# Kernel optimization log

Hardware: AMD Instinct MI355X
Metric: run time of the kernel (lower is better)

## Reference

```python
import jax, jax.numpy as jnp
import numpy as np

N = 25000      # nodes
E = 400000     # edges (before self loops)
G = 64         # graphs in batch
H = 16         # attention heads
ITER = 10      # stacked main GATv2 layers


def setup_inputs():
    key = jax.random.key(0)
    c = [0]
    def nk():
        c[0] += 1
        return jax.random.fold_in(key, c[0])
    def glorot(shape):
        fan = shape[-2] + shape[-1]
        return jax.random.normal(nk(), shape, jnp.float32) * np.float32(np.sqrt(2.0 / fan))
    inp = {
        "x": jax.random.normal(nk(), (N, 2), jnp.float32),
        "edge_attr": jax.random.normal(nk(), (E, 2), jnp.float32),
        "edge_index": jax.random.randint(nk(), (2, E), 0, N, jnp.int32),
        "mask": jax.random.randint(nk(), (N,), 0, 2, jnp.int32),
        "batch": jnp.sort(jax.random.randint(nk(), (N,), 0, G, jnp.int32)),
        # gcn: GATv2Conv(2, 4, heads=16, edge_dim=2), concat -> 64
        "g0_Wl": glorot((2, 64)), "g0_bl": jnp.zeros((64,), jnp.float32),
        "g0_Wr": glorot((2, 64)), "g0_br": jnp.zeros((64,), jnp.float32),
        "g0_We": glorot((2, 64)), "g0_att": glorot((H, 4)),
        "g0_bias": jnp.zeros((64,), jnp.float32),
        "bn_gamma": jnp.ones((64,), jnp.float32),
        "bn_beta": jnp.zeros((64,), jnp.float32),
        "m_Wl": glorot((ITER, 64, 64)), "m_bl": jnp.zeros((ITER, 64), jnp.float32),
        "m_Wr": glorot((ITER, 64, 64)), "m_br": jnp.zeros((ITER, 64), jnp.float32),
        "m_We": glorot((ITER, 2, 64)), "m_att": glorot((ITER, H, 4)),
        "m_bias": jnp.zeros((ITER, 64), jnp.float32),
        # final: GATv2Conv(64, 1, heads=16, concat=False)
        "f_Wl": glorot((64, 16)), "f_bl": jnp.zeros((16,), jnp.float32),
        "f_Wr": glorot((64, 16)), "f_br": jnp.zeros((16,), jnp.float32),
        "f_We": glorot((2, 16)), "f_att": glorot((H, 1)),
        "f_bias": jnp.zeros((1,), jnp.float32),
        # sbs: GATv2Conv(64, 1, heads=16, concat=False)
        "s_Wl": glorot((64, 16)), "s_bl": jnp.zeros((16,), jnp.float32),
        "s_Wr": glorot((64, 16)), "s_br": jnp.zeros((16,), jnp.float32),
        "s_We": glorot((2, 16)), "s_att": glorot((H, 1)),
        "s_bias": jnp.zeros((1,), jnp.float32),
    }
    return inp


def _gatv2(x, src, dst, eattr, Wl, bl, Wr, br, We, att, bias, concat):
    """PyG GATv2Conv: x_l[j]+x_r[i]+e -> LeakyReLU(0.2) -> att dot -> segment softmax over dst."""
    n = x.shape[0]
    h, c = att.shape
    xl = (x @ Wl + bl).reshape(n, h, c)
    xr = (x @ Wr + br).reshape(n, h, c)
    e = (eattr @ We).reshape(-1, h, c)
    m = jax.nn.leaky_relu(xl[src] + xr[dst] + e, 0.2)          # [Etot,H,C]
    logit = jnp.einsum('ehc,hc->eh', m, att)                    # [Etot,H]
    lmax = jax.ops.segment_max(logit, dst, num_segments=n)
    ex = jnp.exp(logit - lmax[dst])
    den = jax.ops.segment_sum(ex, dst, num_segments=n)
    alpha = ex / den[dst]
    out = jax.ops.segment_sum(xl[src] * alpha[..., None], dst, num_segments=n)  # [N,H,C]
    out = out.reshape(n, h * c) if concat else out.mean(axis=1)
    return out + bias


def reference(x, edge_attr, edge_index, mask, batch,
              g0_Wl, g0_bl, g0_Wr, g0_br, g0_We, g0_att, g0_bias,
              bn_gamma, bn_beta,
              m_Wl, m_bl, m_Wr, m_br, m_We, m_att, m_bias,
              f_Wl, f_bl, f_Wr, f_br, f_We, f_att, f_bias,
              s_Wl, s_bl, s_Wr, s_br, s_We, s_att, s_bias):
    n = x.shape[0]
    src, dst = edge_index[0], edge_index[1]
    # add self loops; self-loop edge attr = mean of incoming edge attrs (fill_value='mean')
    ones = jnp.ones((src.shape[0],), jnp.float32)
    cnt = jax.ops.segment_sum(ones, dst, num_segments=n)
    esum = jax.ops.segment_sum(edge_attr, dst, num_segments=n)
    loop_attr = esum / jnp.maximum(cnt, 1.0)[:, None]
    arng = jnp.arange(n, dtype=edge_index.dtype)
    src2 = jnp.concatenate([src, arng])
    dst2 = jnp.concatenate([dst, arng])
    ea2 = jnp.concatenate([edge_attr, loop_attr], axis=0)

    h0 = _gatv2(x, src2, dst2, ea2, g0_Wl, g0_bl, g0_Wr, g0_br, g0_We, g0_att, g0_bias, True)
    mu = h0.mean(axis=0)
    var = h0.var(axis=0)
    h = jax.nn.leaky_relu((h0 - mu) * jax.lax.rsqrt(var + 1e-5) * bn_gamma + bn_beta, 0.01)

    def step(hc, p):
        Wl, bl, Wr, br, We, att, bias = p
        hc = jax.nn.leaky_relu(_gatv2(hc, src2, dst2, ea2, Wl, bl, Wr, br, We, att, bias, True), 0.01)
        return hc, None
    h, _ = jax.lax.scan(step, h, (m_Wl, m_bl, m_Wr, m_br, m_We, m_att, m_bias))

    mus = _gatv2(h, src2, dst2, ea2, s_Wl, s_bl, s_Wr, s_br, s_We, s_att, s_bias, False)[:, 0]  # [N]
    fin = _gatv2(h, src2, dst2, ea2, f_Wl, f_bl, f_Wr, f_br, f_We, f_att, f_bias, False)        # [N,1]
    w = (mask == 0).astype(jnp.float32)
    sums = jax.ops.segment_sum(fin * w[:, None], batch, num_segments=G)
    cnts = jax.ops.segment_sum(w, batch, num_segments=G)
    sat = (sums / jnp.maximum(cnts, 1.0)[:, None])[:, 0]  # [G]
    return mus, sat
```

## Files before the change

### kernel.cpp

```cpp
#include <hip/hip_runtime.h>


static __device__ __forceinline__ float lrelu(float x, float s) {
    return x > 0.f ? x : s * x;
}

__global__ void k_build0(const int* __restrict__ dst, int* __restrict__ cnt,
                         int* __restrict__ rank, int E,
                         const float* __restrict__ x,
                         const float* __restrict__ Wl, const float* __restrict__ bl,
                         const float* __restrict__ Wr, const float* __restrict__ br,
                         float* __restrict__ xl, float* __restrict__ xr, int n) {
    int idx = blockIdx.x * blockDim.x + threadIdx.x;
    if (idx < E) {
        rank[idx] = atomicAdd(&cnt[dst[idx]], 1);
    } else {
        int t = idx - E;
        if (t < n * 64) {
            int i = t >> 6, c = t & 63;
            float x0 = x[2 * i], x1 = x[2 * i + 1];
            xl[t] = x0 * Wl[c] + x1 * Wl[64 + c] + bl[c];
            xr[t] = x0 * Wr[c] + x1 * Wr[64 + c] + br[c];
        }
    }
}

__global__ void k_segoff(const int* __restrict__ cnt, int* __restrict__ row_start,
                         int* __restrict__ cursor, int n) {
    int i = blockIdx.x * blockDim.x + threadIdx.x;
    int lane = threadIdx.x & 63;
    int v = (i < n) ? cnt[i] + 1 : 0;
    int s = v;
#pragma unroll
    for (int off = 1; off < 64; off <<= 1) {
        int t = __shfl_up(s, off);
        if (lane >= off) s += t;
    }
    int wavetot = __shfl(s, 63);
    int base = 0;
    if (lane == 63) base = atomicAdd(cursor, wavetot);
    base = __shfl(base, 63);
    if (i < n) row_start[i] = base + s - v;
}

__global__ void k_scatter(const int* __restrict__ src, const int* __restrict__ dst,
                          const float* __restrict__ ea, const int* __restrict__ rank,
                          const int* __restrict__ row_start,
                          int* __restrict__ csr_src, float* __restrict__ csr_ea, int E) {
    int e = blockIdx.x * blockDim.x + threadIdx.x;
    if (e >= E) return;
    int pos = row_start[dst[e]] + rank[e];
    csr_src[pos] = src[e];
    *(float2*)(csr_ea + 2 * (size_t)pos) = *(const float2*)(ea + 2 * (size_t)e);
}

__global__ void k_selfloop(const int* __restrict__ row_start, const int* __restrict__ cnt,
                           int* __restrict__ csr_src, float* __restrict__ csr_ea, int n) {
    int i = blockIdx.x * blockDim.x + threadIdx.x;
    if (i >= n) return;
    int p0 = row_start[i], deg = cnt[i];
    float s0 = 0.f, s1 = 0.f;
    for (int p = p0; p < p0 + deg; ++p) {
        s0 += csr_ea[2 * (size_t)p];
        s1 += csr_ea[2 * (size_t)p + 1];
    }
    float c = fmaxf((float)deg, 1.f);
    int pl = p0 + deg;
    csr_src[pl] = i;
    csr_ea[2 * (size_t)pl] = s0 / c;
    csr_ea[2 * (size_t)pl + 1] = s1 / c;
}

__launch_bounds__(256)
__global__ void k_proj64(const float* __restrict__ h,
                         const float* __restrict__ Wl, const float* __restrict__ bl,
                         const float* __restrict__ Wr, const float* __restrict__ br,
                         const double* __restrict__ stats,
                         const float* __restrict__ bng, const float* __restrict__ bnb,
                         float* __restrict__ xl, float* __restrict__ xr, int n) {
    __shared__ float wsl[4096], wsr[4096], bna[64], bnbb[64];
    int t = threadIdx.x;
    for (int i = t; i < 4096; i += 256) { wsl[i] = Wl[i]; wsr[i] = Wr[i]; }
    const bool bn = (stats != nullptr);
    if (bn && t < 64) {
        double mu = stats[t] / n;
        double var = stats[64 + t] / n - mu * mu;
        float rs = (float)(1.0 / sqrt(var + 1e-5));
        float a = rs * bng[t];
        bna[t] = a;
        bnbb[t] = bnb[t] - (float)mu * a;
    }
    __syncthreads();
    int rg = t >> 2, cg4 = (t & 3) << 4;
    int r0 = blockIdx.x * 128 + rg * 2;
    float accl[2][16], accr[2][16];
#pragma unroll
    for (int r = 0; r < 2; ++r)
#pragma unroll
        for (int j = 0; j < 16; ++j) { accl[r][j] = 0.f; accr[r][j] = 0.f; }
    for (int k0 = 0; k0 < 64; k0 += 4) {
        float hk[2][4];
#pragma unroll
        for (int r = 0; r < 2; ++r) {
            int gr = r0 + r;
            float4 v = (gr < n) ? *(const float4*)(h + (size_t)gr * 64 + k0)
                                : make_float4(0.f, 0.f, 0.f, 0.f);
            hk[r][0] = v.x; hk[r][1] = v.y; hk[r][2] = v.z; hk[r][3] = v.w;
            if (bn) {
#pragma unroll
                for (int kk = 0; kk < 4; ++kk)
                    hk[r][kk] = lrelu(hk[r][kk] * bna[k0 + kk] + bnbb[k0 + kk], 0.01f);
            }
        }
#pragma unroll
        for (int kk = 0; kk < 4; ++kk) {
            const float* wl = wsl + (k0 + kk) * 64 + cg4;
            const float* wr = wsr + (k0 + kk) * 64 + cg4;
#pragma unroll
            for (int r = 0; r < 2; ++r)
#pragma unroll
                for (int j = 0; j < 16; ++j) {
                    accl[r][j] += hk[r][kk] * wl[j];
                    accr[r][j] += hk[r][kk] * wr[j];
                }
        }
    }
#pragma unroll
    for (int r = 0; r < 2; ++r) {
        int gr = r0 + r;
        if (gr < n) {
            float* ol = xl + (size_t)gr * 64 + cg4;
            float* orr = xr + (size_t)gr * 64 + cg4;
#pragma unroll
            for (int j = 0; j < 16; ++j) {
                ol[j] = accl[r][j] + bl[cg4 + j];
                orr[j] = accr[r][j] + br[cg4 + j];
            }
        }
    }
}

__launch_bounds__(256)
__global__ void k_proj_final(const float* __restrict__ h,
                             const float* __restrict__ fWl, const float* __restrict__ fbl,
                             const float* __restrict__ fWr, const float* __restrict__ fbr,
                             const float* __restrict__ sWl, const float* __restrict__ sbl,
                             const float* __restrict__ sWr, const float* __restrict__ sbr,
                             float* __restrict__ packed, int n) {
    __shared__ float ws[4096];
    __shared__ float bs[64];
    int t = threadIdx.x;
    for (int i = t; i < 1024; i += 256) {
        int k = i >> 4, j = i & 15;
        ws[k * 64 + j] = fWl[i];
        ws[k * 64 + 16 + j] = sWl[i];
        ws[k * 64 + 32 + j] = fWr[i];
        ws[k * 64 + 48 + j] = sWr[i];
    }
    if (t < 16) { bs[t] = fbl[t]; bs[16 + t] = sbl[t]; bs[32 + t] = fbr[t]; bs[48 + t] = sbr[t]; }
    __syncthreads();
    int rg = t >> 2, cg4 = (t & 3) << 4;
    int r0 = blockIdx.x * 256 + rg * 4;
    float acc[4][16];
#pragma unroll
    for (int r = 0; r < 4; ++r)
#pragma unroll
        for (int j = 0; j < 16; ++j) acc[r][j] = 0.f;
    for (int k0 = 0; k0 < 64; k0 += 4) {
        float hk[4][4];
#pragma unroll
        for (int r = 0; r < 4; ++r) {
            int gr = r0 + r;
            float4 v = (gr < n) ? *(const float4*)(h + (size_t)gr * 64 + k0)
                                : make_float4(0.f, 0.f, 0.f, 0.f);
            hk[r][0] = v.x; hk[r][1] = v.y; hk[r][2] = v.z; hk[r][3] = v.w;
        }
#pragma unroll
        for (int kk = 0; kk < 4; ++kk) {
            const float* wrow = ws + (k0 + kk) * 64 + cg4;
#pragma unroll
            for (int r = 0; r < 4; ++r)
#pragma unroll
                for (int j = 0; j < 16; ++j) acc[r][j] += hk[r][kk] * wrow[j];
        }
    }
#pragma unroll
    for (int r = 0; r < 4; ++r) {
        int gr = r0 + r;
        if (gr < n) {
            float* o = packed + (size_t)gr * 64 + cg4;
#pragma unroll
            for (int j = 0; j < 16; ++j) o[j] = acc[r][j] + bs[cg4 + j];
        }
    }
}

__launch_bounds__(256)
__global__ void k_gat(const float* __restrict__ xl, const float* __restrict__ xr,
                      const int* __restrict__ row_start, const int* __restrict__ cnt,
                      const int* __restrict__ csr_src, const float* __restrict__ csr_ea,
                      const float* __restrict__ We, const float* __restrict__ att,
                      const float* __restrict__ bias,
                      float* __restrict__ out, int n, int relu) {
    int wave = (blockIdx.x * blockDim.x + threadIdx.x) >> 6;
    int lane = threadIdx.x & 63;
    if (wave >= n) return;
    const int d = wave;
    const int p0 = __builtin_amdgcn_readfirstlane(row_start[d]);
    const int p1 = p0 + __builtin_amdgcn_readfirstlane(cnt[d]) + 1;
    const float we0 = We[lane], we1 = We[64 + lane];
    const float av = att[lane];
    const float xrv = xr[(size_t)d * 64 + lane];

    float mx0 = -3.0e38f, den0 = 0.f, acc0 = 0.f;
    float mx1 = -3.0e38f, den1 = 0.f, acc1 = 0.f;

    auto step = [&](float xv, float2 ea, bool valid, float& mx, float& den, float& acc) {
        float tv = lrelu(xv + xrv + ea.x * we0 + ea.y * we1, 0.2f) * av;
        tv += __shfl_xor(tv, 1);
        tv += __shfl_xor(tv, 2);
        if (!valid) tv = -__builtin_inff();
        float nm = fmaxf(mx, tv);
        float sc = __expf(mx - nm), w = __expf(tv - nm);
        den = den * sc + w;
        acc = acc * sc + w * xv;
        mx = nm;
    };

    for (int p = p0; p < p1; p += 4) {
        int q1 = min(p + 1, p1 - 1), q2 = min(p + 2, p1 - 1), q3 = min(p + 3, p1 - 1);
        int s0 = csr_src[p], s1 = csr_src[q1], s2 = csr_src[q2], s3 = csr_src[q3];
        float2 e0 = *(const float2*)(csr_ea + 2 * (size_t)p);
        float2 e1 = *(const float2*)(csr_ea + 2 * (size_t)q1);
        float2 e2 = *(const float2*)(csr_ea + 2 * (size_t)q2);
        float2 e3 = *(const float2*)(csr_ea + 2 * (size_t)q3);
        float x0 = xl[(size_t)s0 * 64 + lane];
        float x1 = xl[(size_t)s1 * 64 + lane];
        float x2 = xl[(size_t)s2 * 64 + lane];
        float x3 = xl[(size_t)s3 * 64 + lane];
        step(x0, e0, true, mx0, den0, acc0);
        step(x1, e1, p + 1 < p1, mx1, den1, acc1);
        step(x2, e2, p + 2 < p1, mx0, den0, acc0);
        step(x3, e3, p + 3 < p1, mx1, den1, acc1);
    }
    float nm = fmaxf(mx0, mx1);
    float sc0 = __expf(mx0 - nm), sc1 = __expf(mx1 - nm);
    float o = (acc0 * sc0 + acc1 * sc1) / (den0 * sc0 + den1 * sc1) + bias[lane];
    if (relu) o = lrelu(o, 0.01f);
    out[(size_t)d * 64 + lane] = o;
}

__launch_bounds__(256)
__global__ void k_gat_final(const float* __restrict__ packed,
                            const int* __restrict__ row_start, const int* __restrict__ cnt,
                            const int* __restrict__ csr_src, const float* __restrict__ csr_ea,
                            const float* __restrict__ fWe, const float* __restrict__ sWe,
                            const float* __restrict__ fatt, const float* __restrict__ satt,
                            const float* __restrict__ fbias, const float* __restrict__ sbias,
                            float* __restrict__ fin, float* __restrict__ mus, int n) {
    int hw = (blockIdx.x * blockDim.x + threadIdx.x) >> 5;
    if (hw >= n) return;
    int l = threadIdx.x & 31;
    int hh = l & 15, sel = l >> 4;
    const int d = hw;
    const int p0 = row_start[d], p1 = p0 + cnt[d] + 1;
    const float* We = sel ? sWe : fWe;
    float we0 = We[hh], we1 = We[16 + hh];
    float av = (sel ? satt : fatt)[hh];
    float xrv = packed[(size_t)d * 64 + 32 + sel * 16 + hh];
    int xli = sel * 16 + hh;

    float mx0 = -3.0e38f, den0 = 0.f, acc0 = 0.f;
    float mx1 = -3.0e38f, den1 = 0.f, acc1 = 0.f;

    auto step = [&](float xv, float2 ea, bool valid, float& mx, float& den, float& acc) {
        float t = lrelu(xv + xrv + ea.x * we0 + ea.y * we1, 0.2f) * av;
        if (!valid) t = -__builtin_inff();
        float nm = fmaxf(mx, t);
        float sc = __expf(mx - nm), w = __expf(t - nm);
        den = den * sc + w;
        acc = acc * sc + w * xv;
        mx = nm;
    };

    for (int p = p0; p < p1; p += 4) {
        int q1 = min(p + 1, p1 - 1), q2 = min(p + 2, p1 - 1), q3 = min(p + 3, p1 - 1);
        int s0 = csr_src[p], s1 = csr_src[q1], s2 = csr_src[q2], s3 = csr_src[q3];
        float2 e0 = *(const float2*)(csr_ea + 2 * (size_t)p);
        float2 e1 = *(const float2*)(csr_ea + 2 * (size_t)q1);
        float2 e2 = *(const float2*)(csr_ea + 2 * (size_t)q2);
        float2 e3 = *(const float2*)(csr_ea + 2 * (size_t)q3);
        float x0 = packed[(size_t)s0 * 64 + xli];
        float x1 = packed[(size_t)s1 * 64 + xli];
        float x2 = packed[(size_t)s2 * 64 + xli];
        float x3 = packed[(size_t)s3 * 64 + xli];
        step(x0, e0, true, mx0, den0, acc0);
        step(x1, e1, p + 1 < p1, mx1, den1, acc1);
        step(x2, e2, p + 2 < p1, mx0, den0, acc0);
        step(x3, e3, p + 3 < p1, mx1, den1, acc1);
    }
    float nm = fmaxf(mx0, mx1);
    float s0 = __expf(mx0 - nm), s1 = __expf(mx1 - nm);
    float val = (acc0 * s0 + acc1 * s1) / (den0 * s0 + den1 * s1);
#pragma unroll
    for (int w = 1; w < 16; w <<= 1) val += __shfl_xor(val, w);
    if ((threadIdx.x & 15) == 0) {
        float o = val * (1.f / 16.f) + (sel ? sbias[0] : fbias[0]);
        if (sel) mus[d] = o; else fin[d] = o;
    }
}


__global__ void k_bnstats(const float* __restrict__ h, double* __restrict__ stats, int n) {
    int c = threadIdx.x & 63;
    int s0 = blockIdx.x * (blockDim.x >> 6) + (threadIdx.x >> 6);
    int ns = gridDim.x * (blockDim.x >> 6);
    double s = 0.0, s2 = 0.0;
    for (int i = s0; i < n; i += ns) {
        float v = h[(size_t)i * 64 + c];
        s += v;
        s2 += (double)v * v;
    }
    atomicAdd(&stats[c], s);
    atomicAdd(&stats[64 + c], s2);
}


__global__ void k_sat_acc(const float* __restrict__ fin, const int* __restrict__ mask,
                          const int* __restrict__ batch,
                          float* __restrict__ sums, float* __restrict__ cnts, int n) {
    int i = blockIdx.x * blockDim.x + threadIdx.x;
    int lane = threadIdx.x & 63;
    int g = (i < n) ? batch[i] : -1;
    float c = (i < n && mask[i] == 0) ? 1.f : 0.f;
    float v = (c > 0.f) ? fin[i] : 0.f;
#pragma unroll
    for (int off = 1; off < 64; off <<= 1) {
        float v2 = __shfl_down(v, off);
        float c2 = __shfl_down(c, off);
        int g2 = __shfl_down(g, off);
        if (lane + off < 64 && g2 == g) { v += v2; c += c2; }
    }
    int gprev = __shfl_up(g, 1);
    bool head = (lane == 0) || (gprev != g);
    if (head && g >= 0 && c > 0.f) {
        atomicAdd(&sums[g], v);
        atomicAdd(&cnts[g], c);
    }
}

__global__ void k_sat_fin(const float* __restrict__ sums, const float* __restrict__ cnts,
                          float* __restrict__ out, int g) {
    int i = threadIdx.x;
    if (i < g) out[i] = sums[i] / fmaxf(cnts[i], 1.f);
}


extern "C" void kernel_launch(void* const* d_in, const int* in_sizes, int n_in,
                              void* d_out, int out_size, void* d_ws, size_t ws_size,
                              hipStream_t stream) {
    const float* x = (const float*)d_in[0];
    const float* eat = (const float*)d_in[1];
    const int* ei = (const int*)d_in[2];
    const int* mask = (const int*)d_in[3];
    const int* batch = (const int*)d_in[4];
    const float* g0_Wl = (const float*)d_in[5];
    const float* g0_bl = (const float*)d_in[6];
    const float* g0_Wr = (const float*)d_in[7];
    const float* g0_br = (const float*)d_in[8];
    const float* g0_We = (const float*)d_in[9];
    const float* g0_att = (const float*)d_in[10];
    const float* g0_bias = (const float*)d_in[11];
    const float* bn_g = (const float*)d_in[12];
    const float* bn_b = (const float*)d_in[13];
    const float* m_Wl = (const float*)d_in[14];
    const float* m_bl = (const float*)d_in[15];
    const float* m_Wr = (const float*)d_in[16];
    const float* m_br = (const float*)d_in[17];
    const float* m_We = (const float*)d_in[18];
    const float* m_att = (const float*)d_in[19];
    const float* m_bias = (const float*)d_in[20];
    const float* f_Wl = (const float*)d_in[21];
    const float* f_bl = (const float*)d_in[22];
    const float* f_Wr = (const float*)d_in[23];
    const float* f_br = (const float*)d_in[24];
    const float* f_We = (const float*)d_in[25];
    const float* f_att = (const float*)d_in[26];
    const float* f_bias = (const float*)d_in[27];
    const float* s_Wl = (const float*)d_in[28];
    const float* s_bl = (const float*)d_in[29];
    const float* s_Wr = (const float*)d_in[30];
    const float* s_br = (const float*)d_in[31];
    const float* s_We = (const float*)d_in[32];
    const float* s_att = (const float*)d_in[33];
    const float* s_bias = (const float*)d_in[34];

    const int N = in_sizes[3];
    const int E = in_sizes[1] / 2;
    const int G = out_size - N;
    const int ITER = in_sizes[14] / 4096;
    const int ET = E + N;
    const int* srcp = ei;
    const int* dstp = ei + E;

    char* wsb = (char*)d_ws;
    size_t off = 0;
    auto alloc = [&](size_t b) { void* p = wsb + off; off = (off + b + 255) & ~(size_t)255; return p; };
    int* cnt = (int*)alloc((size_t)N * 4);
    int* cursor = (int*)alloc(256);
    double* stats = (double*)alloc(128 * 8);
    float* sums = (float*)alloc((size_t)G * 4);
    float* cnts = (float*)alloc((size_t)G * 4);
    size_t zero_bytes = off;
    int* rank = (int*)alloc((size_t)E * 4);
    int* row_start = (int*)alloc((size_t)N * 4);
    int* csr_src = (int*)alloc((size_t)ET * 4);
    float* csr_ea = (float*)alloc((size_t)ET * 8);
    float* xl = (float*)alloc((size_t)N * 256);
    float* xr = (float*)alloc((size_t)N * 256);
    float* hbuf = (float*)alloc((size_t)N * 256);
    float* fin = (float*)alloc((size_t)N * 4);
    (void)ws_size; (void)n_in;

    float* outv = (float*)d_out;

    hipMemsetAsync(d_ws, 0, zero_bytes, stream);
    const int tb = 256;
    k_build0<<<(E + N * 64 + tb - 1) / tb, tb, 0, stream>>>(dstp, cnt, rank, E,
                                                            x, g0_Wl, g0_bl, g0_Wr, g0_br,
                                                            xl, xr, N);
    k_segoff<<<(N + tb - 1) / tb, tb, 0, stream>>>(cnt, row_start, cursor, N);
    k_scatter<<<(E + tb - 1) / tb, tb, 0, stream>>>(srcp, dstp, eat, rank, row_start,
                                                    csr_src, csr_ea, E);
    k_selfloop<<<(N + tb - 1) / tb, tb, 0, stream>>>(row_start, cnt, csr_src, csr_ea, N);

    k_gat<<<(N * 64 + tb - 1) / tb, tb, 0, stream>>>(xl, xr, row_start, cnt, csr_src, csr_ea,
                                                     g0_We, g0_att, g0_bias, hbuf, N, 0);
    k_bnstats<<<128, 256, 0, stream>>>(hbuf, stats, N);

    int gp = (N + 127) / 128;
    for (int l = 0; l < ITER; ++l) {
        k_proj64<<<gp, 256, 0, stream>>>(hbuf, m_Wl + (size_t)l * 4096, m_bl + l * 64,
                                         m_Wr + (size_t)l * 4096, m_br + l * 64,
                                         (l == 0) ? stats : nullptr, bn_g, bn_b,
                                         xl, xr, N);
        k_gat<<<(N * 64 + tb - 1) / tb, tb, 0, stream>>>(xl, xr, row_start, cnt, csr_src, csr_ea,
                                                         m_We + l * 128, m_att + l * 64,
                                                         m_bias + l * 64, hbuf, N, 1);
    }
    k_proj_final<<<(N + 255) / 256, 256, 0, stream>>>(hbuf, f_Wl, f_bl, f_Wr, f_br,
                                                      s_Wl, s_bl, s_Wr, s_br, xl, N);
    k_gat_final<<<(N * 32 + tb - 1) / tb, tb, 0, stream>>>(xl, row_start, cnt, csr_src, csr_ea,
                                                           f_We, s_We, f_att, s_att,
                                                           f_bias, s_bias, fin, outv, N);
    k_sat_acc<<<(N + tb - 1) / tb, tb, 0, stream>>>(fin, mask, batch, sums, cnts, N);
    k_sat_fin<<<1, 64, 0, stream>>>(sums, cnts, outv + N, G);
}
```

Baseline: 744.8 us.

## Fuse next-layer projection into GAT aggregation kernel with ping-pong buffers

Each main-layer GAT aggregation kernel now also computes the next layer's Wl/Wr projection in-register: each wave broadcasts its node's output across lanes with shuffles and multiplies by weights read from global memory. The last layer fuses the final/sbs projection instead. This removes the separate projection launches and the round trip of the hidden state through global memory, and double-buffers xl/xr so a layer never overwrites the inputs its neighbours still read. In exchange, weights are read per wave from global/cache rather than shared memory, and each wave now does 64-step shuffle loops after its aggregation.

```diff
diff --git a/kernel.cpp b/kernel.cpp
--- a/kernel.cpp
+++ b/kernel.cpp
@@ -81,8 +81,7 @@
     __shared__ float wsl[4096], wsr[4096], bna[64], bnbb[64];
     int t = threadIdx.x;
     for (int i = t; i < 4096; i += 256) { wsl[i] = Wl[i]; wsr[i] = Wr[i]; }
-    const bool bn = (stats != nullptr);
-    if (bn && t < 64) {
+    if (t < 64) {
         double mu = stats[t] / n;
         double var = stats[64 + t] / n - mu * mu;
         float rs = (float)(1.0 / sqrt(var + 1e-5));
@@ -106,11 +105,9 @@
             float4 v = (gr < n) ? *(const float4*)(h + (size_t)gr * 64 + k0)
                                 : make_float4(0.f, 0.f, 0.f, 0.f);
             hk[r][0] = v.x; hk[r][1] = v.y; hk[r][2] = v.z; hk[r][3] = v.w;
-            if (bn) {
-#pragma unroll
-                for (int kk = 0; kk < 4; ++kk)
-                    hk[r][kk] = lrelu(hk[r][kk] * bna[k0 + kk] + bnbb[k0 + kk], 0.01f);
-            }
+#pragma unroll
+            for (int kk = 0; kk < 4; ++kk)
+                hk[r][kk] = lrelu(hk[r][kk] * bna[k0 + kk] + bnbb[k0 + kk], 0.01f);
         }
 #pragma unroll
         for (int kk = 0; kk < 4; ++kk) {
@@ -140,72 +137,16 @@
     }
 }
 
-__launch_bounds__(256)
-__global__ void k_proj_final(const float* __restrict__ h,
-                             const float* __restrict__ fWl, const float* __restrict__ fbl,
-                             const float* __restrict__ fWr, const float* __restrict__ fbr,
-                             const float* __restrict__ sWl, const float* __restrict__ sbl,
-                             const float* __restrict__ sWr, const float* __restrict__ sbr,
-                             float* __restrict__ packed, int n) {
-    __shared__ float ws[4096];
-    __shared__ float bs[64];
-    int t = threadIdx.x;
-    for (int i = t; i < 1024; i += 256) {
-        int k = i >> 4, j = i & 15;
-        ws[k * 64 + j] = fWl[i];
-        ws[k * 64 + 16 + j] = sWl[i];
-        ws[k * 64 + 32 + j] = fWr[i];
-        ws[k * 64 + 48 + j] = sWr[i];
-    }
-    if (t < 16) { bs[t] = fbl[t]; bs[16 + t] = sbl[t]; bs[32 + t] = fbr[t]; bs[48 + t] = sbr[t]; }
-    __syncthreads();
-    int rg = t >> 2, cg4 = (t & 3) << 4;
-    int r0 = blockIdx.x * 256 + rg * 4;
-    float acc[4][16];
-#pragma unroll
-    for (int r = 0; r < 4; ++r)
-#pragma unroll
-        for (int j = 0; j < 16; ++j) acc[r][j] = 0.f;
-    for (int k0 = 0; k0 < 64; k0 += 4) {
-        float hk[4][4];
-#pragma unroll
-        for (int r = 0; r < 4; ++r) {
-            int gr = r0 + r;
-            float4 v = (gr < n) ? *(const float4*)(h + (size_t)gr * 64 + k0)
-                                : make_float4(0.f, 0.f, 0.f, 0.f);
-            hk[r][0] = v.x; hk[r][1] = v.y; hk[r][2] = v.z; hk[r][3] = v.w;
-        }
-#pragma unroll
-        for (int kk = 0; kk < 4; ++kk) {
-            const float* wrow = ws + (k0 + kk) * 64 + cg4;
-#pragma unroll
-            for (int r = 0; r < 4; ++r)
-#pragma unroll
-                for (int j = 0; j < 16; ++j) acc[r][j] += hk[r][kk] * wrow[j];
-        }
-    }
-#pragma unroll
-    for (int r = 0; r < 4; ++r) {
-        int gr = r0 + r;
-        if (gr < n) {
-            float* o = packed + (size_t)gr * 64 + cg4;
-#pragma unroll
-            for (int j = 0; j < 16; ++j) o[j] = acc[r][j] + bs[cg4 + j];
-        }
-    }
-}
-
-__launch_bounds__(256)
-__global__ void k_gat(const float* __restrict__ xl, const float* __restrict__ xr,
-                      const int* __restrict__ row_start, const int* __restrict__ cnt,
-                      const int* __restrict__ csr_src, const float* __restrict__ csr_ea,
-                      const float* __restrict__ We, const float* __restrict__ att,
-                      const float* __restrict__ bias,
-                      float* __restrict__ out, int n, int relu) {
-    int wave = (blockIdx.x * blockDim.x + threadIdx.x) >> 6;
-    int lane = threadIdx.x & 63;
-    if (wave >= n) return;
-    const int d = wave;
+__device__ __forceinline__ float gat_node(const float* __restrict__ xl,
+                                          const float* __restrict__ xr,
+                                          const int* __restrict__ row_start,
+                                          const int* __restrict__ cnt,
+                                          const int* __restrict__ csr_src,
+                                          const float* __restrict__ csr_ea,
+                                          const float* __restrict__ We,
+                                          const float* __restrict__ att,
+                                          const float* __restrict__ bias,
+                                          int d, int lane, int relu) {
     const int p0 = __builtin_amdgcn_readfirstlane(row_start[d]);
     const int p1 = p0 + __builtin_amdgcn_readfirstlane(cnt[d]) + 1;
     const float we0 = We[lane], we1 = We[64 + lane];
@@ -247,7 +188,77 @@
     float sc0 = __expf(mx0 - nm), sc1 = __expf(mx1 - nm);
     float o = (acc0 * sc0 + acc1 * sc1) / (den0 * sc0 + den1 * sc1) + bias[lane];
     if (relu) o = lrelu(o, 0.01f);
-    out[(size_t)d * 64 + lane] = o;
+    return o;
+}
+
+__launch_bounds__(256)
+__global__ void k_gat(const float* __restrict__ xl, const float* __restrict__ xr,
+                      const int* __restrict__ row_start, const int* __restrict__ cnt,
+                      const int* __restrict__ csr_src, const float* __restrict__ csr_ea,
+                      const float* __restrict__ We, const float* __restrict__ att,
+                      const float* __restrict__ bias,
+                      float* __restrict__ out, int n, int relu) {
+    int wave = (blockIdx.x * blockDim.x + threadIdx.x) >> 6;
+    int lane = threadIdx.x & 63;
+    if (wave >= n) return;
+    float o = gat_node(xl, xr, row_start, cnt, csr_src, csr_ea, We, att, bias, wave, lane, relu);
+    out[(size_t)wave * 64 + lane] = o;
+}
+
+__launch_bounds__(256)
+__global__ void k_gat_proj(const float* __restrict__ xl, const float* __restrict__ xr,
+                           const int* __restrict__ row_start, const int* __restrict__ cnt,
+                           const int* __restrict__ csr_src, const float* __restrict__ csr_ea,
+                           const float* __restrict__ We, const float* __restrict__ att,
+                           const float* __restrict__ bias,
+                           const float* __restrict__ Wnl, const float* __restrict__ bnl,
+                           const float* __restrict__ Wnr, const float* __restrict__ bnr,
+                           float* __restrict__ xl_out, float* __restrict__ xr_out, int n) {
+    int wave = (blockIdx.x * blockDim.x + threadIdx.x) >> 6;
+    int lane = threadIdx.x & 63;
+    if (wave >= n) return;
+    const int d = wave;
+    float o = gat_node(xl, xr, row_start, cnt, csr_src, csr_ea, We, att, bias, d, lane, 1);
+    float a0 = 0.f, a1 = 0.f, b0 = 0.f, b1 = 0.f;
+#pragma unroll 8
+    for (int k = 0; k < 64; k += 2) {
+        float h0 = __shfl(o, k);
+        float h1 = __shfl(o, k + 1);
+        a0 += h0 * Wnl[k * 64 + lane];
+        a1 += h1 * Wnl[(k + 1) * 64 + lane];
+        b0 += h0 * Wnr[k * 64 + lane];
+        b1 += h1 * Wnr[(k + 1) * 64 + lane];
+    }
+    xl_out[(size_t)d * 64 + lane] = a0 + a1 + bnl[lane];
+    xr_out[(size_t)d * 64 + lane] = b0 + b1 + bnr[lane];
+}
+
+__launch_bounds__(256)
+__global__ void k_gat_projfin(const float* __restrict__ xl, const float* __restrict__ xr,
+                              const int* __restrict__ row_start, const int* __restrict__ cnt,
+                              const int* __restrict__ csr_src, const float* __restrict__ csr_ea,
+                              const float* __restrict__ We, const float* __restrict__ att,
+                              const float* __restrict__ bias,
+                              const float* __restrict__ fWl, const float* __restrict__ fbl,
+                              const float* __restrict__ fWr, const float* __restrict__ fbr,
+                              const float* __restrict__ sWl, const float* __restrict__ sbl,
+                              const float* __restrict__ sWr, const float* __restrict__ sbr,
+                              float* __restrict__ packed, int n) {
+    int wave = (blockIdx.x * blockDim.x + threadIdx.x) >> 6;
+    int lane = threadIdx.x & 63;
+    if (wave >= n) return;
+    const int d = wave;
+    float o = gat_node(xl, xr, row_start, cnt, csr_src, csr_ea, We, att, bias, d, lane, 1);
+    int q = lane >> 4, cc = lane & 15;
+    const float* W = (q == 0) ? fWl : (q == 1) ? sWl : (q == 2) ? fWr : sWr;
+    const float* B = (q == 0) ? fbl : (q == 1) ? sbl : (q == 2) ? fbr : sbr;
+    float a0 = 0.f, a1 = 0.f;
+#pragma unroll 8
+    for (int k = 0; k < 64; k += 2) {
+        a0 += __shfl(o, k) * W[k * 16 + cc];
+        a1 += __shfl(o, k + 1) * W[(k + 1) * 16 + cc];
+    }
+    packed[(size_t)d * 64 + lane] = a0 + a1 + B[cc];
 }
 
 __launch_bounds__(256)
@@ -416,8 +427,10 @@
     int* row_start = (int*)alloc((size_t)N * 4);
     int* csr_src = (int*)alloc((size_t)ET * 4);
     float* csr_ea = (float*)alloc((size_t)ET * 8);
-    float* xl = (float*)alloc((size_t)N * 256);
-    float* xr = (float*)alloc((size_t)N * 256);
+    float* xlA = (float*)alloc((size_t)N * 256);
+    float* xrA = (float*)alloc((size_t)N * 256);
+    float* xlB = (float*)alloc((size_t)N * 256);
+    float* xrB = (float*)alloc((size_t)N * 256);
     float* hbuf = (float*)alloc((size_t)N * 256);
     float* fin = (float*)alloc((size_t)N * 4);
     (void)ws_size; (void)n_in;
@@ -426,31 +439,42 @@
 
     hipMemsetAsync(d_ws, 0, zero_bytes, stream);
     const int tb = 256;
+    const int ggrid = (N * 64 + tb - 1) / tb;
     k_build0<<<(E + N * 64 + tb - 1) / tb, tb, 0, stream>>>(dstp, cnt, rank, E,
                                                             x, g0_Wl, g0_bl, g0_Wr, g0_br,
-                                                            xl, xr, N);
+                                                            xlA, xrA, N);
     k_segoff<<<(N + tb - 1) / tb, tb, 0, stream>>>(cnt, row_start, cursor, N);
     k_scatter<<<(E + tb - 1) / tb, tb, 0, stream>>>(srcp, dstp, eat, rank, row_start,
                                                     csr_src, csr_ea, E);
     k_selfloop<<<(N + tb - 1) / tb, tb, 0, stream>>>(row_start, cnt, csr_src, csr_ea, N);
 
-    k_gat<<<(N * 64 + tb - 1) / tb, tb, 0, stream>>>(xl, xr, row_start, cnt, csr_src, csr_ea,
-                                                     g0_We, g0_att, g0_bias, hbuf, N, 0);
+    k_gat<<<ggrid, tb, 0, stream>>>(xlA, xrA, row_start, cnt, csr_src, csr_ea,
+                                    g0_We, g0_att, g0_bias, hbuf, N, 0);
     k_bnstats<<<128, 256, 0, stream>>>(hbuf, stats, N);
-
-    int gp = (N + 127) / 128;
+    k_proj64<<<(N + 127) / 128, 256, 0, stream>>>(hbuf, m_Wl, m_bl, m_Wr, m_br,
+                                                  stats, bn_g, bn_b, xlA, xrA, N);
+
+    float* cur_l = xlA; float* cur_r = xrA;
+    float* alt_l = xlB; float* alt_r = xrB;
     for (int l = 0; l < ITER; ++l) {
-        k_proj64<<<gp, 256, 0, stream>>>(hbuf, m_Wl + (size_t)l * 4096, m_bl + l * 64,
-                                         m_Wr + (size_t)l * 4096, m_br + l * 64,
-                                         (l == 0) ? stats : nullptr, bn_g, bn_b,
-                                         xl, xr, N);
-        k_gat<<<(N * 64 + tb - 1) / tb, tb, 0, stream>>>(xl, xr, row_start, cnt, csr_src, csr_ea,
-                                                         m_We + l * 128, m_att + l * 64,
-                                                         m_bias + l * 64, hbuf, N, 1);
-    }
-    k_proj_final<<<(N + 255) / 256, 256, 0, stream>>>(hbuf, f_Wl, f_bl, f_Wr, f_br,
-                                                      s_Wl, s_bl, s_Wr, s_br, xl, N);
-    k_gat_final<<<(N * 32 + tb - 1) / tb, tb, 0, stream>>>(xl, row_start, cnt, csr_src, csr_ea,
+        if (l < ITER - 1) {
+            k_gat_proj<<<ggrid, tb, 0, stream>>>(cur_l, cur_r, row_start, cnt, csr_src, csr_ea,
+                                                 m_We + l * 128, m_att + l * 64, m_bias + l * 64,
+                                                 m_Wl + (size_t)(l + 1) * 4096, m_bl + (l + 1) * 64,
+                                                 m_Wr + (size_t)(l + 1) * 4096, m_br + (l + 1) * 64,
+                                                 alt_l, alt_r, N);
+        } else {
+            k_gat_projfin<<<ggrid, tb, 0, stream>>>(cur_l, cur_r, row_start, cnt, csr_src, csr_ea,
+                                                    m_We + l * 128, m_att + l * 64, m_bias + l * 64,
+                                                    f_Wl, f_bl, f_Wr, f_br,
+                                                    s_Wl, s_bl, s_Wr, s_br,
+                                                    alt_l, N);
+        }
+        float* t;
+        t = cur_l; cur_l = alt_l; alt_l = t;
+        t = cur_r; cur_r = alt_r; alt_r = t;
+    }
+    k_gat_final<<<(N * 32 + tb - 1) / tb, tb, 0, stream>>>(cur_l, row_start, cnt, csr_src, csr_ea,
                                                            f_We, s_We, f_att, s_att,
                                                            f_bias, s_bias, fin, outv, N);
     k_sat_acc<<<(N + tb - 1) / tb, tb, 0, stream>>>(fin, mask, batch, sums, cnts, N);
```

Measured after the change: 675.1 us. -9.3%, faster.
